# Performance work log

Measured on AMD Instinct MI355X. Metric: run time of the kernel, lower is better.

The kernel has to match this reference:

```python
import jax, jax.numpy as jnp
import numpy as np

WS = 7           # window size
N = WS * WS      # tokens per window = 49
C = 128          # embed dim
H = 4            # heads
HD = C // H      # head dim = 32
NW = 64          # num windows (mask leading dim)
B = 4096         # total windows = outer_batch * NW


def _relative_indexes():
    ch = np.arange(WS)
    cw = np.arange(WS)
    coords = np.stack(np.meshgrid(ch, cw, indexing='ij')).reshape(2, -1)  # [2, N]
    rel = coords[:, :, None] - coords[:, None, :]                          # [2, N, N]
    rel = rel.transpose(1, 2, 0)
    rel[:, :, 0] += WS - 1
    rel[:, :, 1] += WS - 1
    rel[:, :, 0] *= 2 * WS - 1
    return jnp.asarray(rel.sum(-1), dtype=jnp.int32)                       # [N, N]


def setup_inputs() -> dict:
    key = jax.random.key(0)
    ks = jax.random.split(key, 10)
    s = 0.02
    return {
        'query': jax.random.normal(ks[0], (B, N, C), jnp.float32),
        'source': jax.random.normal(ks[1], (B, N, C), jnp.float32),
        'mask': jnp.zeros((NW, N, N), jnp.float32),
        'q_w': jax.random.normal(ks[2], (C, C), jnp.float32) * s,
        'q_b': jnp.zeros((C,), jnp.float32),
        'kv_w': jax.random.normal(ks[3], (C, 2 * C), jnp.float32) * s,
        'kv_b': jnp.zeros((2 * C,), jnp.float32),
        'proj_w': jax.random.normal(ks[4], (C, C), jnp.float32) * s,
        'proj_b': jnp.zeros((C,), jnp.float32),
        'bias_table': jax.random.normal(ks[5], ((2 * WS - 1) ** 2, H), jnp.float32) * s,
        'rel_idx': _relative_indexes(),
    }


def reference(query, source, mask, q_w, q_b, kv_w, kv_b, proj_w, proj_b, bias_table, rel_idx):
    scale = HD ** -0.5
    q = query @ q_w + q_b                       # [B, N, C]
    kv = source @ kv_w + kv_b                   # [B, N, 2C]
    k, v = kv[..., :C], kv[..., C:]
    # [B, N, H, HD] -> [B, H, N, HD]
    q = q.reshape(B, N, H, HD).transpose(0, 2, 1, 3) * scale
    k = k.reshape(B, N, H, HD).transpose(0, 2, 1, 3)
    v = v.reshape(B, N, H, HD).transpose(0, 2, 1, 3)
    attn = jnp.einsum('bhnd,bhmd->bhnm', q, k)  # [B, H, N, N]
    # gathered relative positional bias: [1, H, N, N]
    bias = bias_table[rel_idx.reshape(-1)].reshape(N, N, H).transpose(2, 0, 1)[None]
    attn = attn + bias
    # mask: [NW, N, N] broadcast over outer batch and heads
    attn = attn.reshape(-1, NW, H, N, N) + mask[None, :, None]
    attn = attn.reshape(B, H, N, N)
    attn = jax.nn.softmax(attn, axis=-1)
    x = jnp.einsum('bhnm,bhmd->bnhd', attn, v).reshape(B, N, C)
    return x @ proj_w + proj_b
```

## Files before the change

kernel.cpp:

```cpp
#include <hip/hip_runtime.h>

#define NN 49
#define CC 128
#define HH 4
#define NWIN 64
#define BB 4096
#define QSCALE 0.17677669529663687f

typedef __attribute__((ext_vector_type(8))) short bf16x8;
typedef __attribute__((ext_vector_type(4))) float f32x4;
typedef unsigned short u16;
typedef unsigned int u32;

__device__ __forceinline__ u16 f2b(float f) {
    u32 x = __float_as_uint(f);
    return (u16)((x + 0x7fffu + ((x >> 16) & 1u)) >> 16);
}
__device__ __forceinline__ float b2f(u16 u) { return __uint_as_float(((u32)u) << 16); }
__device__ __forceinline__ uint2 pack4(float a, float b, float c, float d) {
    uint2 r;
    r.x = (u32)f2b(a) | ((u32)f2b(b) << 16);
    r.y = (u32)f2b(c) | ((u32)f2b(d) << 16);
    return r;
}
__device__ __forceinline__ f32x4 mfma16(bf16x8 a, bf16x8 b, f32x4 c) {
    return __builtin_amdgcn_mfma_f32_16x16x32_bf16(a, b, c, 0, 0, 0);
}
__device__ __forceinline__ char* adr256(u16* base, int row, int byte) {
    return (char*)base + row * 256 + (byte ^ ((row & 7) << 4));
}
__device__ __forceinline__ char* adr128(u16* base, int row, int byte) {
    return (char*)base + row * 128 + (byte ^ ((row & 7) << 4));
}

__global__ void prep_cbt(const float* __restrict__ bias_table, const int* __restrict__ rel_idx,
                         const float* __restrict__ mask, u16* __restrict__ cbt) {
    int idx = blockIdx.x * blockDim.x + threadIdx.x;
    int m = idx & 63, i = (idx >> 6) & 63, h = (idx >> 12) & 3, wv = idx >> 14;
    if (wv >= NWIN) return;
    float v = -1e9f;
    if (m < NN && i < NN)
        v = bias_table[rel_idx[i * NN + m] * HH + h] + mask[(wv * NN + i) * NN + m];
    cbt[idx] = f2b(v);
}

__global__ void prep_w(const float* __restrict__ qw, const float* __restrict__ qb,
                       const float* __restrict__ kvw, const float* __restrict__ pjw,
                       u16* __restrict__ qwp, u16* __restrict__ kvwp,
                       u16* __restrict__ pjwp, float* __restrict__ qbs) {
    int idx = blockIdx.x * blockDim.x + threadIdx.x;
    if (idx < 16384) {
        int i = idx & 7, lane = (idx >> 3) & 63, kt = (idx >> 9) & 3, nt = idx >> 11;
        int k = 32 * kt + 8 * (lane >> 4) + i, n = 16 * nt + (lane & 15);
        qwp[idx] = f2b(qw[k * CC + n] * QSCALE);
    } else if (idx < 49152) {
        int j = idx - 16384;
        int i = j & 7, lane = (j >> 3) & 63, kt = (j >> 9) & 3, nt = j >> 11;
        int k = 32 * kt + 8 * (lane >> 4) + i, n = 16 * nt + (lane & 15);
        kvwp[j] = f2b(kvw[k * 2 * CC + n]);
    } else if (idx < 65536) {
        int j = idx - 49152;
        int i = j & 7, lane = (j >> 3) & 63, kt = (j >> 9) & 3, nt = j >> 11;
        int k = 32 * kt + 8 * (lane >> 4) + i, n = 16 * nt + (lane & 15);
        pjwp[j] = f2b(pjw[k * CC + n]);
    } else if (idx < 65664) {
        int j = idx - 65536;
        qbs[j] = qb[j] * QSCALE;
    }
}

__global__ __launch_bounds__(256, 2)
void wmha_main(const float* __restrict__ query, const float* __restrict__ source,
               const u16* __restrict__ qwp, const u16* __restrict__ kvwp,
               const u16* __restrict__ pjwp, const float* __restrict__ qbs,
               const float* __restrict__ kv_b, const float* __restrict__ proj_b,
               const u16* __restrict__ cbt, float* __restrict__ out) {
    __shared__ u16 lds[32768];
    u16* R0 = lds;
    u16* R1 = lds + 8192;
    u16* R2 = lds + 16384;
    u16* R3 = lds + 24576;
    const int t = threadIdx.x;
    const int b = blockIdx.x;
    const int w = t >> 6, lane = t & 63;
    const int lq = lane & 15, qd = lane >> 4;

    {
        const int row = t >> 2, qu = t & 3;
        const size_t gbase = (size_t)b * NN * CC + row * CC + qu * 32;
        #pragma unroll
        for (int j = 0; j < 4; ++j) {
            bf16x8 vq = {0,0,0,0,0,0,0,0}, vs = {0,0,0,0,0,0,0,0};
            if (row < NN) {
                const float4* q4 = (const float4*)(query + gbase) + 2 * j;
                const float4* s4 = (const float4*)(source + gbase) + 2 * j;
                float4 a0 = q4[0], a1 = q4[1], c0 = s4[0], c1 = s4[1];
                vq[0]=(short)f2b(a0.x); vq[1]=(short)f2b(a0.y); vq[2]=(short)f2b(a0.z); vq[3]=(short)f2b(a0.w);
                vq[4]=(short)f2b(a1.x); vq[5]=(short)f2b(a1.y); vq[6]=(short)f2b(a1.z); vq[7]=(short)f2b(a1.w);
                vs[0]=(short)f2b(c0.x); vs[1]=(short)f2b(c0.y); vs[2]=(short)f2b(c0.z); vs[3]=(short)f2b(c0.w);
                vs[4]=(short)f2b(c1.x); vs[5]=(short)f2b(c1.y); vs[6]=(short)f2b(c1.z); vs[7]=(short)f2b(c1.w);
            }
            *(bf16x8*)adr256(R0, row, qu * 64 + 16 * j) = vq;
            *(bf16x8*)adr256(R1, row, qu * 64 + 16 * j) = vs;
        }
    }
    __syncthreads();

    {
        bf16x8 bw[2][4];
        #pragma unroll
        for (int n2 = 0; n2 < 2; ++n2)
            #pragma unroll
            for (int kt = 0; kt < 4; ++kt)
                bw[n2][kt] = *(const bf16x8*)(qwp + (((w + 4 * n2) * 4 + kt) * 64 + lane) * 8);
        f32x4 acc[4][2] = {};
        #pragma unroll
        for (int mt = 0; mt < 4; ++mt) {
            bf16x8 a[4];
            #pragma unroll
            for (int kt = 0; kt < 4; ++kt)
                a[kt] = *(const bf16x8*)adr256(R0, mt * 16 + lq, kt * 64 + qd * 16);
            #pragma unroll
            for (int n2 = 0; n2 < 2; ++n2)
                #pragma unroll
                for (int kt = 0; kt < 4; ++kt)
                    acc[mt][n2] = mfma16(a[kt], bw[n2][kt], acc[mt][n2]);
        }
        #pragma unroll
        for (int n2 = 0; n2 < 2; ++n2) {
            const int col = 16 * (w + 4 * n2) + lq;
            const float bias = qbs[col];
            #pragma unroll
            for (int mt = 0; mt < 4; ++mt)
                #pragma unroll
                for (int r = 0; r < 4; ++r) {
                    const int row = mt * 16 + qd * 4 + r;
                    *(u16*)adr256(R2, row, 2 * col) = f2b(acc[mt][n2][r] + bias);
                }
        }
    }

    {
        bf16x8 bw[4][4];
        #pragma unroll
        for (int n4 = 0; n4 < 4; ++n4)
            #pragma unroll
            for (int kt = 0; kt < 4; ++kt)
                bw[n4][kt] = *(const bf16x8*)(kvwp + (((w + 4 * n4) * 4 + kt) * 64 + lane) * 8);
        f32x4 acc[4][4] = {};
        #pragma unroll
        for (int mt = 0; mt < 4; ++mt) {
            bf16x8 a[4];
            #pragma unroll
            for (int kt = 0; kt < 4; ++kt)
                a[kt] = *(const bf16x8*)adr256(R1, mt * 16 + lq, kt * 64 + qd * 16);
            #pragma unroll
            for (int n4 = 0; n4 < 4; ++n4)
                #pragma unroll
                for (int kt = 0; kt < 4; ++kt)
                    acc[mt][n4] = mfma16(a[kt], bw[n4][kt], acc[mt][n4]);
        }
        #pragma unroll
        for (int n4 = 0; n4 < 2; ++n4) {
            const int col = 16 * (w + 4 * n4) + lq;
            const float bias = kv_b[col];
            #pragma unroll
            for (int mt = 0; mt < 4; ++mt)
                #pragma unroll
                for (int r = 0; r < 4; ++r) {
                    const int row = mt * 16 + qd * 4 + r;
                    *(u16*)adr256(R3, row, 2 * col) = f2b(acc[mt][n4][r] + bias);
                }
        }
        __syncthreads();
        #pragma unroll
        for (int n4 = 2; n4 < 4; ++n4) {
            const int dim = 16 * w + 64 * (n4 - 2) + lq;
            const float bias = kv_b[CC + dim];
            #pragma unroll
            for (int mt = 0; mt < 4; ++mt) {
                uint2 pk = pack4(acc[mt][n4][0] + bias, acc[mt][n4][1] + bias,
                                 acc[mt][n4][2] + bias, acc[mt][n4][3] + bias);
                *(uint2*)adr128(R1, dim, 2 * (mt * 16 + qd * 4)) = pk;
            }
        }
    }

    const int h = w;
    f32x4 s[4][4];
    uint2 cb2[4][4];
    float inv[4];
    u16* ph = (w < 2 ? R0 : R2) + (w & 1) * 4096;
    {
        bf16x8 kf[4], qf[4];
        #pragma unroll
        for (int a = 0; a < 4; ++a)
            kf[a] = *(const bf16x8*)adr256(R3, a * 16 + lq, h * 64 + qd * 16);
        #pragma unroll
        for (int bq = 0; bq < 4; ++bq)
            qf[bq] = *(const bf16x8*)adr256(R2, bq * 16 + lq, h * 64 + qd * 16);
        const u16* cbb = cbt + (((size_t)((b & (NWIN - 1)) * HH + h)) << 12);
        #pragma unroll
        for (int bq = 0; bq < 4; ++bq)
            #pragma unroll
            for (int a = 0; a < 4; ++a)
                cb2[bq][a] = *(const uint2*)(cbb + (bq * 16 + lq) * 64 + a * 16 + qd * 4);
        #pragma unroll
        for (int bq = 0; bq < 4; ++bq) {
            f32x4 z = {0.f, 0.f, 0.f, 0.f};
            #pragma unroll
            for (int a = 0; a < 4; ++a)
                s[bq][a] = mfma16(kf[a], qf[bq], z);
        }
    }
    __syncthreads();

    #pragma unroll
    for (int bq = 0; bq < 4; ++bq) {
        #pragma unroll
        for (int a = 0; a < 4; ++a) {
            s[bq][a][0] += b2f((u16)(cb2[bq][a].x & 0xffffu));
            s[bq][a][1] += b2f((u16)(cb2[bq][a].x >> 16));
            s[bq][a][2] += b2f((u16)(cb2[bq][a].y & 0xffffu));
            s[bq][a][3] += b2f((u16)(cb2[bq][a].y >> 16));
        }
        float m0 = s[bq][0][0];
        #pragma unroll
        for (int a = 0; a < 4; ++a)
            #pragma unroll
            for (int r = 0; r < 4; ++r) m0 = fmaxf(m0, s[bq][a][r]);
        m0 = fmaxf(m0, __shfl_xor(m0, 16));
        m0 = fmaxf(m0, __shfl_xor(m0, 32));
        float sm = 0.f;
        const int prow = bq * 16 + lq;
        #pragma unroll
        for (int a = 0; a < 4; ++a) {
            u16 p0 = f2b(__expf(s[bq][a][0] - m0));
            u16 p1 = f2b(__expf(s[bq][a][1] - m0));
            u16 p2 = f2b(__expf(s[bq][a][2] - m0));
            u16 p3 = f2b(__expf(s[bq][a][3] - m0));
            sm += b2f(p0) + b2f(p1) + b2f(p2) + b2f(p3);
            uint2 pk;
            pk.x = (u32)p0 | ((u32)p1 << 16);
            pk.y = (u32)p2 | ((u32)p3 << 16);
            *(uint2*)adr128(ph, prow, 2 * (a * 16 + qd * 4)) = pk;
        }
        sm += __shfl_xor(sm, 16);
        sm += __shfl_xor(sm, 32);
        inv[bq] = 1.f / sm;
    }

    {
        f32x4 o[2][4] = {};
        bf16x8 vf[2][2];
        #pragma unroll
        for (int dt = 0; dt < 2; ++dt)
            #pragma unroll
            for (int kt = 0; kt < 2; ++kt)
                vf[dt][kt] = *(const bf16x8*)adr128(R1, h * 32 + dt * 16 + lq, kt * 64 + qd * 16);
        #pragma unroll
        for (int bq = 0; bq < 4; ++bq)
            #pragma unroll
            for (int kt = 0; kt < 2; ++kt) {
                bf16x8 pf = *(const bf16x8*)adr128(ph, bq * 16 + lq, kt * 64 + qd * 16);
                #pragma unroll
                for (int dt = 0; dt < 2; ++dt)
                    o[dt][bq] = mfma16(vf[dt][kt], pf, o[dt][bq]);
            }
        #pragma unroll
        for (int bq = 0; bq < 4; ++bq)
            #pragma unroll
            for (int dt = 0; dt < 2; ++dt) {
                const int row = bq * 16 + lq;
                uint2 pk = pack4(o[dt][bq][0] * inv[bq], o[dt][bq][1] * inv[bq],
                                 o[dt][bq][2] * inv[bq], o[dt][bq][3] * inv[bq]);
                *(uint2*)adr256(R3, row, 2 * (h * 32 + dt * 16 + qd * 4)) = pk;
            }
    }

    {
        bf16x8 bw[2][4];
        #pragma unroll
        for (int n2 = 0; n2 < 2; ++n2)
            #pragma unroll
            for (int kt = 0; kt < 4; ++kt)
                bw[n2][kt] = *(const bf16x8*)(pjwp + (((w + 4 * n2) * 4 + kt) * 64 + lane) * 8);
        __syncthreads();
        f32x4 acc[4][2] = {};
        #pragma unroll
        for (int mt = 0; mt < 4; ++mt) {
            bf16x8 a[4];
            #pragma unroll
            for (int kt = 0; kt < 4; ++kt)
                a[kt] = *(const bf16x8*)adr256(R3, mt * 16 + lq, kt * 64 + qd * 16);
            #pragma unroll
            for (int n2 = 0; n2 < 2; ++n2)
                #pragma unroll
                for (int kt = 0; kt < 4; ++kt)
                    acc[mt][n2] = mfma16(a[kt], bw[n2][kt], acc[mt][n2]);
        }
        float* outb = out + (size_t)b * NN * CC;
        #pragma unroll
        for (int n2 = 0; n2 < 2; ++n2) {
            const int col = 16 * (w + 4 * n2) + lq;
            const float bias = proj_b[col];
            #pragma unroll
            for (int mt = 0; mt < 4; ++mt)
                #pragma unroll
                for (int r = 0; r < 4; ++r) {
                    const int row = mt * 16 + qd * 4 + r;
                    if (row < NN) outb[row * CC + col] = acc[mt][n2][r] + bias;
                }
        }
    }
}

extern "C" void kernel_launch(void* const* d_in, const int* in_sizes, int n_in,
                              void* d_out, int out_size, void* d_ws, size_t ws_size,
                              hipStream_t stream) {
    const float* query      = (const float*)d_in[0];
    const float* source     = (const float*)d_in[1];
    const float* mask       = (const float*)d_in[2];
    const float* q_w        = (const float*)d_in[3];
    const float* q_b        = (const float*)d_in[4];
    const float* kv_w       = (const float*)d_in[5];
    const float* kv_b       = (const float*)d_in[6];
    const float* proj_w     = (const float*)d_in[7];
    const float* proj_b     = (const float*)d_in[8];
    const float* bias_table = (const float*)d_in[9];
    const int*   rel_idx    = (const int*)d_in[10];
    float* out = (float*)d_out;

    u16* cbt   = (u16*)d_ws;
    u16* qwp   = cbt + 1048576;
    u16* kvwp  = qwp + 16384;
    u16* pjwp  = kvwp + 32768;
    float* qbs = (float*)(pjwp + 16384);

    prep_cbt<<<4096, 256, 0, stream>>>(bias_table, rel_idx, mask, cbt);
    prep_w<<<257, 256, 0, stream>>>(q_w, q_b, kv_w, proj_w, qwp, kvwp, pjwp, qbs);
    wmha_main<<<BB, 256, 0, stream>>>(query, source, qwp, kvwp, pjwp, qbs,
                                      kv_b, proj_b, cbt, out);
}
```

Measured before the change: 135.7 us.

## Cut LDS to 48KB and split KV GEMM to raise occupancy to 3 blocks

Shared memory is reduced from 64KB to 48KB by reusing three regions instead of four. The KV projection is split into separate K and V passes to halve accumulator registers. Softmax and PV now run per 16-row query tile with a small per-wave P buffer, and launch bounds move to 3 blocks per CU. s_setprio hints are wrapped around the MFMA loops. This targets low occupancy and latency hiding, at the cost of an extra barrier, re-reading source tiles from LDS, and tighter register budgets that may spill.

```diff
diff --git a/kernel.cpp b/kernel.cpp
--- a/kernel.cpp
+++ b/kernel.cpp
@@ -69,17 +69,16 @@
     }
 }
 
-__global__ __launch_bounds__(256, 2)
+__global__ __launch_bounds__(256, 3)
 void wmha_main(const float* __restrict__ query, const float* __restrict__ source,
                const u16* __restrict__ qwp, const u16* __restrict__ kvwp,
                const u16* __restrict__ pjwp, const float* __restrict__ qbs,
                const float* __restrict__ kv_b, const float* __restrict__ proj_b,
                const u16* __restrict__ cbt, float* __restrict__ out) {
-    __shared__ u16 lds[32768];
+    __shared__ u16 lds[24576];
     u16* R0 = lds;
     u16* R1 = lds + 8192;
     u16* R2 = lds + 16384;
-    u16* R3 = lds + 24576;
     const int t = threadIdx.x;
     const int b = blockIdx.x;
     const int w = t >> 6, lane = t & 63;
@@ -101,19 +100,20 @@
                 vs[4]=(short)f2b(c1.x); vs[5]=(short)f2b(c1.y); vs[6]=(short)f2b(c1.z); vs[7]=(short)f2b(c1.w);
             }
             *(bf16x8*)adr256(R0, row, qu * 64 + 16 * j) = vq;
-            *(bf16x8*)adr256(R1, row, qu * 64 + 16 * j) = vs;
-        }
-    }
+            *(bf16x8*)adr256(R2, row, qu * 64 + 16 * j) = vs;
+        }
+    }
+    bf16x8 bwq[2][4];
+    #pragma unroll
+    for (int n2 = 0; n2 < 2; ++n2)
+        #pragma unroll
+        for (int kt = 0; kt < 4; ++kt)
+            bwq[n2][kt] = *(const bf16x8*)(qwp + (((w + 4 * n2) * 4 + kt) * 64 + lane) * 8);
     __syncthreads();
 
     {
-        bf16x8 bw[2][4];
-        #pragma unroll
-        for (int n2 = 0; n2 < 2; ++n2)
-            #pragma unroll
-            for (int kt = 0; kt < 4; ++kt)
-                bw[n2][kt] = *(const bf16x8*)(qwp + (((w + 4 * n2) * 4 + kt) * 64 + lane) * 8);
         f32x4 acc[4][2] = {};
+        __builtin_amdgcn_s_setprio(1);
         #pragma unroll
         for (int mt = 0; mt < 4; ++mt) {
             bf16x8 a[4];
@@ -124,8 +124,9 @@
             for (int n2 = 0; n2 < 2; ++n2)
                 #pragma unroll
                 for (int kt = 0; kt < 4; ++kt)
-                    acc[mt][n2] = mfma16(a[kt], bw[n2][kt], acc[mt][n2]);
-        }
+                    acc[mt][n2] = mfma16(a[kt], bwq[n2][kt], acc[mt][n2]);
+        }
+        __builtin_amdgcn_s_setprio(0);
         #pragma unroll
         for (int n2 = 0; n2 < 2; ++n2) {
             const int col = 16 * (w + 4 * n2) + lq;
@@ -135,147 +136,169 @@
                 #pragma unroll
                 for (int r = 0; r < 4; ++r) {
                     const int row = mt * 16 + qd * 4 + r;
-                    *(u16*)adr256(R2, row, 2 * col) = f2b(acc[mt][n2][r] + bias);
+                    *(u16*)adr256(R1, row, 2 * col) = f2b(acc[mt][n2][r] + bias);
                 }
         }
     }
-
-    {
-        bf16x8 bw[4][4];
-        #pragma unroll
-        for (int n4 = 0; n4 < 4; ++n4)
-            #pragma unroll
-            for (int kt = 0; kt < 4; ++kt)
-                bw[n4][kt] = *(const bf16x8*)(kvwp + (((w + 4 * n4) * 4 + kt) * 64 + lane) * 8);
-        f32x4 acc[4][4] = {};
+    __syncthreads();
+
+    {
+        bf16x8 bw[2][4];
+        #pragma unroll
+        for (int n2 = 0; n2 < 2; ++n2)
+            #pragma unroll
+            for (int kt = 0; kt < 4; ++kt)
+                bw[n2][kt] = *(const bf16x8*)(kvwp + (((w + 4 * n2) * 4 + kt) * 64 + lane) * 8);
+        f32x4 acc[4][2] = {};
+        __builtin_amdgcn_s_setprio(1);
         #pragma unroll
         for (int mt = 0; mt < 4; ++mt) {
             bf16x8 a[4];
             #pragma unroll
             for (int kt = 0; kt < 4; ++kt)
-                a[kt] = *(const bf16x8*)adr256(R1, mt * 16 + lq, kt * 64 + qd * 16);
-            #pragma unroll
-            for (int n4 = 0; n4 < 4; ++n4)
+                a[kt] = *(const bf16x8*)adr256(R2, mt * 16 + lq, kt * 64 + qd * 16);
+            #pragma unroll
+            for (int n2 = 0; n2 < 2; ++n2)
                 #pragma unroll
                 for (int kt = 0; kt < 4; ++kt)
-                    acc[mt][n4] = mfma16(a[kt], bw[n4][kt], acc[mt][n4]);
-        }
-        #pragma unroll
-        for (int n4 = 0; n4 < 2; ++n4) {
-            const int col = 16 * (w + 4 * n4) + lq;
+                    acc[mt][n2] = mfma16(a[kt], bw[n2][kt], acc[mt][n2]);
+        }
+        __builtin_amdgcn_s_setprio(0);
+        #pragma unroll
+        for (int n2 = 0; n2 < 2; ++n2) {
+            const int col = 16 * (w + 4 * n2) + lq;
             const float bias = kv_b[col];
             #pragma unroll
             for (int mt = 0; mt < 4; ++mt)
                 #pragma unroll
                 for (int r = 0; r < 4; ++r) {
                     const int row = mt * 16 + qd * 4 + r;
-                    *(u16*)adr256(R3, row, 2 * col) = f2b(acc[mt][n4][r] + bias);
+                    *(u16*)adr256(R0, row, 2 * col) = f2b(acc[mt][n2][r] + bias);
                 }
         }
+    }
+
+    {
+        bf16x8 bw[2][4];
+        #pragma unroll
+        for (int n2 = 0; n2 < 2; ++n2)
+            #pragma unroll
+            for (int kt = 0; kt < 4; ++kt)
+                bw[n2][kt] = *(const bf16x8*)(kvwp + (((w + 8 + 4 * n2) * 4 + kt) * 64 + lane) * 8);
+        f32x4 acc[4][2] = {};
+        __builtin_amdgcn_s_setprio(1);
+        #pragma unroll
+        for (int mt = 0; mt < 4; ++mt) {
+            bf16x8 a[4];
+            #pragma unroll
+            for (int kt = 0; kt < 4; ++kt)
+                a[kt] = *(const bf16x8*)adr256(R2, mt * 16 + lq, kt * 64 + qd * 16);
+            #pragma unroll
+            for (int n2 = 0; n2 < 2; ++n2)
+                #pragma unroll
+                for (int kt = 0; kt < 4; ++kt)
+                    acc[mt][n2] = mfma16(a[kt], bw[n2][kt], acc[mt][n2]);
+        }
+        __builtin_amdgcn_s_setprio(0);
         __syncthreads();
         #pragma unroll
-        for (int n4 = 2; n4 < 4; ++n4) {
-            const int dim = 16 * w + 64 * (n4 - 2) + lq;
+        for (int n2 = 0; n2 < 2; ++n2) {
+            const int dim = 16 * w + 64 * n2 + lq;
             const float bias = kv_b[CC + dim];
             #pragma unroll
             for (int mt = 0; mt < 4; ++mt) {
-                uint2 pk = pack4(acc[mt][n4][0] + bias, acc[mt][n4][1] + bias,
-                                 acc[mt][n4][2] + bias, acc[mt][n4][3] + bias);
-                *(uint2*)adr128(R1, dim, 2 * (mt * 16 + qd * 4)) = pk;
+                uint2 pk = pack4(acc[mt][n2][0] + bias, acc[mt][n2][1] + bias,
+                                 acc[mt][n2][2] + bias, acc[mt][n2][3] + bias);
+                *(uint2*)adr128(R2, dim, 2 * (mt * 16 + qd * 4)) = pk;
             }
         }
     }
 
     const int h = w;
     f32x4 s[4][4];
-    uint2 cb2[4][4];
-    float inv[4];
-    u16* ph = (w < 2 ? R0 : R2) + (w & 1) * 4096;
-    {
-        bf16x8 kf[4], qf[4];
+    {
+        bf16x8 kf[4];
         #pragma unroll
         for (int a = 0; a < 4; ++a)
-            kf[a] = *(const bf16x8*)adr256(R3, a * 16 + lq, h * 64 + qd * 16);
-        #pragma unroll
-        for (int bq = 0; bq < 4; ++bq)
-            qf[bq] = *(const bf16x8*)adr256(R2, bq * 16 + lq, h * 64 + qd * 16);
-        const u16* cbb = cbt + (((size_t)((b & (NWIN - 1)) * HH + h)) << 12);
-        #pragma unroll
-        for (int bq = 0; bq < 4; ++bq)
+            kf[a] = *(const bf16x8*)adr256(R0, a * 16 + lq, h * 64 + qd * 16);
+        __builtin_amdgcn_s_setprio(1);
+        #pragma unroll
+        for (int bq = 0; bq < 4; ++bq) {
+            bf16x8 qf = *(const bf16x8*)adr256(R1, bq * 16 + lq, h * 64 + qd * 16);
+            f32x4 z = {0.f, 0.f, 0.f, 0.f};
             #pragma unroll
             for (int a = 0; a < 4; ++a)
-                cb2[bq][a] = *(const uint2*)(cbb + (bq * 16 + lq) * 64 + a * 16 + qd * 4);
+                s[bq][a] = mfma16(kf[a], qf, z);
+        }
+        __builtin_amdgcn_s_setprio(0);
+    }
+    __syncthreads();
+
+    {
+        bf16x8 vf[2][2];
+        #pragma unroll
+        for (int dt = 0; dt < 2; ++dt)
+            #pragma unroll
+            for (int kt = 0; kt < 2; ++kt)
+                vf[dt][kt] = *(const bf16x8*)adr128(R2, h * 32 + dt * 16 + lq, kt * 64 + qd * 16);
+        u16* pb = R0 + w * 1024;
+        const u16* cbb = cbt + ((size_t)((b & (NWIN - 1)) * HH + h) << 12);
         #pragma unroll
         for (int bq = 0; bq < 4; ++bq) {
-            f32x4 z = {0.f, 0.f, 0.f, 0.f};
+            uint2 cb2[4];
             #pragma unroll
             for (int a = 0; a < 4; ++a)
-                s[bq][a] = mfma16(kf[a], qf[bq], z);
-        }
-    }
-    __syncthreads();
-
-    #pragma unroll
-    for (int bq = 0; bq < 4; ++bq) {
-        #pragma unroll
-        for (int a = 0; a < 4; ++a) {
-            s[bq][a][0] += b2f((u16)(cb2[bq][a].x & 0xffffu));
-            s[bq][a][1] += b2f((u16)(cb2[bq][a].x >> 16));
-            s[bq][a][2] += b2f((u16)(cb2[bq][a].y & 0xffffu));
-            s[bq][a][3] += b2f((u16)(cb2[bq][a].y >> 16));
-        }
-        float m0 = s[bq][0][0];
-        #pragma unroll
-        for (int a = 0; a < 4; ++a)
-            #pragma unroll
-            for (int r = 0; r < 4; ++r) m0 = fmaxf(m0, s[bq][a][r]);
-        m0 = fmaxf(m0, __shfl_xor(m0, 16));
-        m0 = fmaxf(m0, __shfl_xor(m0, 32));
-        float sm = 0.f;
-        const int prow = bq * 16 + lq;
-        #pragma unroll
-        for (int a = 0; a < 4; ++a) {
-            u16 p0 = f2b(__expf(s[bq][a][0] - m0));
-            u16 p1 = f2b(__expf(s[bq][a][1] - m0));
-            u16 p2 = f2b(__expf(s[bq][a][2] - m0));
-            u16 p3 = f2b(__expf(s[bq][a][3] - m0));
-            sm += b2f(p0) + b2f(p1) + b2f(p2) + b2f(p3);
-            uint2 pk;
-            pk.x = (u32)p0 | ((u32)p1 << 16);
-            pk.y = (u32)p2 | ((u32)p3 << 16);
-            *(uint2*)adr128(ph, prow, 2 * (a * 16 + qd * 4)) = pk;
-        }
-        sm += __shfl_xor(sm, 16);
-        sm += __shfl_xor(sm, 32);
-        inv[bq] = 1.f / sm;
-    }
-
-    {
-        f32x4 o[2][4] = {};
-        bf16x8 vf[2][2];
-        #pragma unroll
-        for (int dt = 0; dt < 2; ++dt)
-            #pragma unroll
-            for (int kt = 0; kt < 2; ++kt)
-                vf[dt][kt] = *(const bf16x8*)adr128(R1, h * 32 + dt * 16 + lq, kt * 64 + qd * 16);
-        #pragma unroll
-        for (int bq = 0; bq < 4; ++bq)
+                cb2[a] = *(const uint2*)(cbb + (bq * 16 + lq) * 64 + a * 16 + qd * 4);
+            #pragma unroll
+            for (int a = 0; a < 4; ++a) {
+                s[bq][a][0] += b2f((u16)(cb2[a].x & 0xffffu));
+                s[bq][a][1] += b2f((u16)(cb2[a].x >> 16));
+                s[bq][a][2] += b2f((u16)(cb2[a].y & 0xffffu));
+                s[bq][a][3] += b2f((u16)(cb2[a].y >> 16));
+            }
+            float m0 = s[bq][0][0];
+            #pragma unroll
+            for (int a = 0; a < 4; ++a)
+                #pragma unroll
+                for (int r = 0; r < 4; ++r) m0 = fmaxf(m0, s[bq][a][r]);
+            m0 = fmaxf(m0, __shfl_xor(m0, 16));
+            m0 = fmaxf(m0, __shfl_xor(m0, 32));
+            uint2 pk[4];
+            float sm = 0.f;
+            #pragma unroll
+            for (int a = 0; a < 4; ++a) {
+                float p0 = __expf(s[bq][a][0] - m0), p1 = __expf(s[bq][a][1] - m0);
+                float p2 = __expf(s[bq][a][2] - m0), p3 = __expf(s[bq][a][3] - m0);
+                pk[a] = pack4(p0, p1, p2, p3);
+                sm += b2f((u16)pk[a].x) + b2f((u16)(pk[a].x >> 16))
+                    + b2f((u16)pk[a].y) + b2f((u16)(pk[a].y >> 16));
+            }
+            sm += __shfl_xor(sm, 16);
+            sm += __shfl_xor(sm, 32);
+            const float inv = 1.f / sm;
+            #pragma unroll
+            for (int a = 0; a < 4; ++a)
+                *(uint2*)adr128(pb, lq, 32 * a + 8 * qd) = pk[a];
+            asm volatile("s_waitcnt lgkmcnt(0)" ::: "memory");
+            __builtin_amdgcn_sched_barrier(0);
+            f32x4 o[2] = {{0.f,0.f,0.f,0.f},{0.f,0.f,0.f,0.f}};
+            __builtin_amdgcn_s_setprio(1);
             #pragma unroll
             for (int kt = 0; kt < 2; ++kt) {
-                bf16x8 pf = *(const bf16x8*)adr128(ph, bq * 16 + lq, kt * 64 + qd * 16);
+                bf16x8 pf = *(const bf16x8*)adr128(pb, lq, 64 * kt + 16 * qd);
                 #pragma unroll
                 for (int dt = 0; dt < 2; ++dt)
-                    o[dt][bq] = mfma16(vf[dt][kt], pf, o[dt][bq]);
-            }
-        #pragma unroll
-        for (int bq = 0; bq < 4; ++bq)
+                    o[dt] = mfma16(vf[dt][kt], pf, o[dt]);
+            }
+            __builtin_amdgcn_s_setprio(0);
+            __builtin_amdgcn_sched_barrier(0);
             #pragma unroll
             for (int dt = 0; dt < 2; ++dt) {
-                const int row = bq * 16 + lq;
-                uint2 pk = pack4(o[dt][bq][0] * inv[bq], o[dt][bq][1] * inv[bq],
-                                 o[dt][bq][2] * inv[bq], o[dt][bq][3] * inv[bq]);
-                *(uint2*)adr256(R3, row, 2 * (h * 32 + dt * 16 + qd * 4)) = pk;
-            }
+                uint2 px = pack4(o[dt][0] * inv, o[dt][1] * inv,
+                                 o[dt][2] * inv, o[dt][3] * inv);
+                *(uint2*)adr256(R1, bq * 16 + lq, 64 * h + 32 * dt + 8 * qd) = px;
+            }
+        }
     }
 
     {
@@ -287,18 +310,20 @@
                 bw[n2][kt] = *(const bf16x8*)(pjwp + (((w + 4 * n2) * 4 + kt) * 64 + lane) * 8);
         __syncthreads();
         f32x4 acc[4][2] = {};
+        __builtin_amdgcn_s_setprio(1);
         #pragma unroll
         for (int mt = 0; mt < 4; ++mt) {
             bf16x8 a[4];
             #pragma unroll
             for (int kt = 0; kt < 4; ++kt)
-                a[kt] = *(const bf16x8*)adr256(R3, mt * 16 + lq, kt * 64 + qd * 16);
+                a[kt] = *(const bf16x8*)adr256(R1, mt * 16 + lq, kt * 64 + qd * 16);
             #pragma unroll
             for (int n2 = 0; n2 < 2; ++n2)
                 #pragma unroll
                 for (int kt = 0; kt < 4; ++kt)
                     acc[mt][n2] = mfma16(a[kt], bw[n2][kt], acc[mt][n2]);
         }
+        __builtin_amdgcn_s_setprio(0);
         float* outb = out + (size_t)b * NN * CC;
         #pragma unroll
         for (int n2 = 0; n2 < 2; ++n2) {
```

New measurement: 125.3 us. 1.08x faster.
